# Performance work log

Hardware: AMD Instinct MI355X
Metric: run time of the kernel (lower is better)

Reference implementation:

```python
import jax, jax.numpy as jnp
import numpy as np
from jax import lax

B, T, A = 64, 1024, 512
FILTERS, K = 32, 31
PAD = (K - 1) // 2


def setup_inputs() -> dict:
    key = jax.random.key(0)
    ks = jax.random.split(key, 12)
    return {
        "encoder_seq_proj": jax.random.normal(ks[0], (B, T, A), jnp.float32),
        "query": jax.random.normal(ks[1], (B, A), jnp.float32),
        "cumulative": jax.random.uniform(ks[2], (B, T), jnp.float32),
        "attention": jax.random.uniform(ks[3], (B, T), jnp.float32),
        "alpha": jax.random.uniform(ks[4], (B, T), jnp.float32),
        "conv_w": jax.random.normal(ks[5], (FILTERS, 2, K), jnp.float32) * 0.1,
        "L_w": jax.random.normal(ks[6], (A, FILTERS), jnp.float32) * 0.1,
        "L_b": jax.random.normal(ks[7], (A,), jnp.float32) * 0.1,
        "W_w": jax.random.normal(ks[8], (A, A), jnp.float32) * 0.05,
        "W_b": jax.random.normal(ks[9], (A,), jnp.float32) * 0.05,
        "v_w": jax.random.normal(ks[10], (1, A), jnp.float32) * 0.05,
        "t": 1,
        "phone_len": jax.random.randint(ks[11], (B,), 1, T + 1).astype(jnp.int64),
    }


def reference(encoder_seq_proj, query, cumulative, attention, alpha,
              conv_w, L_w, L_b, W_w, W_b, v_w, t, phone_len):
    # attention mask from phone lengths (set at init, reused each step)
    mask = (jnp.arange(T)[None, :] < phone_len[:, None]).astype(encoder_seq_proj.dtype)
    # processed query: [B, 1, A]
    pq = (query @ W_w.T + W_b)[:, None, :]
    # location features: stack cumulative + previous attention -> [B, 2, T]
    loc = jnp.stack([cumulative, attention], axis=1)
    conv_out = lax.conv_general_dilated(
        loc, conv_w, window_strides=(1,), padding=[(PAD, PAD)],
        dimension_numbers=("NCH", "OIH", "NCH"))  # [B, F, T]
    ploc = jnp.einsum("bft,af->bta", conv_out, L_w) + L_b  # [B, T, A]
    # additive energies -> [B, T]
    u = jnp.einsum("bta,a->bt", jnp.tanh(pq + encoder_seq_proj + ploc), v_w[0])
    s = jax.nn.sigmoid(u)
    scores = s / jnp.sum(s, axis=1, keepdims=True)
    att = scores * mask
    # forward-attention recursion (enable_forward_bias=True path)
    shift_alpha = jnp.pad(alpha[:, :-1], ((0, 0), (1, 0)))
    dual_alpha = jnp.pad(alpha[:, :-2], ((0, 0), (2, 0)))
    new_alpha = (shift_alpha + dual_alpha + alpha + 1e-7) * att
    new_alpha = new_alpha / jnp.sum(new_alpha, axis=-1, keepdims=True)
    return new_alpha[:, None, :]  # [B, 1, T]
```

## Files before the change

### kernel.cpp

```cpp
#include <hip/hip_runtime.h>

#define NB 64
#define NT 1024
#define NA 512
#define NF 32
#define KW 31
#define PADW 15
#define TC 64
#define CWN (2 * KW * NF)

typedef __fp16 half2v __attribute__((ext_vector_type(2)));

__device__ __forceinline__ float fast_tanh(float x) {
    float e = __builtin_amdgcn_exp2f(x * 2.885390081777927f);
    return 1.0f - 2.0f * __builtin_amdgcn_rcpf(1.0f + e);
}
__device__ __forceinline__ float fast_sigmoid(float u) {
    return __builtin_amdgcn_rcpf(1.0f + __builtin_amdgcn_exp2f(-u * 1.4426950408889634f));
}
__device__ __forceinline__ unsigned pkrtz(float a, float b) {
    half2v h = __builtin_amdgcn_cvt_pkrtz(a, b);
    return __builtin_bit_cast(unsigned, h);
}
__device__ __forceinline__ float fdot2u(unsigned cv, unsigned lw, float acc) {
#if __has_builtin(__builtin_amdgcn_fdot2)
    return __builtin_amdgcn_fdot2(__builtin_bit_cast(half2v, cv),
                                  __builtin_bit_cast(half2v, lw), acc, false);
#else
    half2v a = __builtin_bit_cast(half2v, cv), b = __builtin_bit_cast(half2v, lw);
    return acc + (float)a.x * (float)b.x + (float)a.y * (float)b.y;
#endif
}

__global__ __launch_bounds__(256) void lsa_pq(
    const float* __restrict__ query, const float* __restrict__ Ww,
    const float* __restrict__ Wb, const float* __restrict__ convw,
    float* __restrict__ pq, float* __restrict__ cwT)
{
    if (blockIdx.x == 0) {
        for (int i = threadIdx.x; i < NF * 2 * KW; i += 256) {
            int f = i / (2 * KW);
            int r = i - f * 2 * KW;
            int c = r / KW;
            int k = r - c * KW;
            cwT[(c * KW + k) * NF + f] = convw[i];
        }
    }
    __shared__ float qs[NA];
    int tid  = threadIdx.x;
    int lane = tid & 63;
    int wv   = tid >> 6;
    int b     = blockIdx.x >> 3;
    int chunk = blockIdx.x & 7;
    qs[tid]       = query[b * NA + tid];
    qs[tid + 256] = query[b * NA + tid + 256];
    __syncthreads();

    float4 q0 = *(const float4*)(qs + 8 * lane);
    float4 q1 = *(const float4*)(qs + 8 * lane + 4);
#pragma unroll 4
    for (int i = 0; i < 16; ++i) {
        int a = chunk * 64 + wv * 16 + i;
        const float4* wr = (const float4*)(Ww + (long)a * NA + 8 * lane);
        float4 w0 = wr[0], w1 = wr[1];
        float s = w0.x * q0.x + w0.y * q0.y + w0.z * q0.z + w0.w * q0.w
                + w1.x * q1.x + w1.y * q1.y + w1.z * q1.z + w1.w * q1.w;
#pragma unroll
        for (int m = 1; m <= 32; m <<= 1) s += __shfl_xor(s, m, 64);
        if (lane == 0) pq[b * NA + a] = s + Wb[a];
    }
}

__global__ __launch_bounds__(256, 4) void lsa_main(
    const float* __restrict__ enc, const float* __restrict__ cum,
    const float* __restrict__ att, const float* __restrict__ cwT,
    const float* __restrict__ Lw, const float* __restrict__ Lb,
    const float* __restrict__ vw, const float* __restrict__ pq,
    float* __restrict__ sout)
{
    __shared__ float cw_s[CWN];
    __shared__ float cum_s[TC + 30];
    __shared__ float att_s[TC + 30];
    __shared__ unsigned cvsh[TC][20];
    __shared__ float wred[4][34];

    int tid  = threadIdx.x;
    int lane = tid & 63;
    int wv   = tid >> 6;
    int b    = blockIdx.x >> 4;
    int t0   = (blockIdx.x & 15) * TC;

    {
        const float4* src = (const float4*)cwT;
        float4* dst = (float4*)cw_s;
        if (tid < 248) {
            dst[tid]       = src[tid];
            dst[tid + 248] = src[tid + 248];
        }
    }
    if (tid < TC + 30) {
        int t = t0 - PADW + tid;
        bool ok = (t >= 0) && (t < NT);
        cum_s[tid] = ok ? cum[b * NT + t] : 0.f;
        att_s[tid] = ok ? att[b * NT + t] : 0.f;
    }

    int a0  = (tid & 127) * 4;
    int tth = tid >> 7;
    unsigned h[4][16];
    float c4[4], v4[4];
#pragma unroll
    for (int ai = 0; ai < 4; ++ai) {
        const float4* lp = (const float4*)(Lw + (long)(a0 + ai) * NF);
#pragma unroll
        for (int i = 0; i < 8; ++i) {
            float4 w = lp[i];
            h[ai][2 * i]     = pkrtz(w.x, w.y);
            h[ai][2 * i + 1] = pkrtz(w.z, w.w);
        }
        c4[ai] = pq[b * NA + a0 + ai] + Lb[a0 + ai];
        v4[ai] = vw[a0 + ai];
    }
    __syncthreads();

    {
        int tt  = lane;
        int fbu = wv * 8;
        float acc[8] = {0, 0, 0, 0, 0, 0, 0, 0};
#pragma unroll
        for (int k = 0; k < KW; ++k) {
            float x0 = cum_s[tt + k];
            float x1 = att_s[tt + k];
            const float4* A  = (const float4*)(cw_s + k * NF + fbu);
            const float4* Bv = (const float4*)(cw_s + (KW + k) * NF + fbu);
#pragma unroll
            for (int j = 0; j < 2; ++j) {
                float4 wa = A[j], wb = Bv[j];
                acc[4 * j + 0] = fmaf(x0, wa.x, fmaf(x1, wb.x, acc[4 * j + 0]));
                acc[4 * j + 1] = fmaf(x0, wa.y, fmaf(x1, wb.y, acc[4 * j + 1]));
                acc[4 * j + 2] = fmaf(x0, wa.z, fmaf(x1, wb.z, acc[4 * j + 2]));
                acc[4 * j + 3] = fmaf(x0, wa.w, fmaf(x1, wb.w, acc[4 * j + 3]));
            }
        }
        uint4 pk;
        pk.x = pkrtz(acc[0], acc[1]);
        pk.y = pkrtz(acc[2], acc[3]);
        pk.z = pkrtz(acc[4], acc[5]);
        pk.w = pkrtz(acc[6], acc[7]);
        *(uint4*)&cvsh[tt][wv * 4] = pk;
    }
    __syncthreads();

#define DOA(ai, ecomp)                                                  \
    {                                                                   \
        float y0 = 0.f, y1 = 0.f;                                       \
        y0 = fdot2u(cva.x, h[ai][0],  y0); y1 = fdot2u(cva.y, h[ai][1],  y1); \
        y0 = fdot2u(cva.z, h[ai][2],  y0); y1 = fdot2u(cva.w, h[ai][3],  y1); \
        y0 = fdot2u(cvb.x, h[ai][4],  y0); y1 = fdot2u(cvb.y, h[ai][5],  y1); \
        y0 = fdot2u(cvb.z, h[ai][6],  y0); y1 = fdot2u(cvb.w, h[ai][7],  y1); \
        y0 = fdot2u(cvc.x, h[ai][8],  y0); y1 = fdot2u(cvc.y, h[ai][9],  y1); \
        y0 = fdot2u(cvc.z, h[ai][10], y0); y1 = fdot2u(cvc.w, h[ai][11], y1); \
        y0 = fdot2u(cvd.x, h[ai][12], y0); y1 = fdot2u(cvd.y, h[ai][13], y1); \
        y0 = fdot2u(cvd.z, h[ai][14], y0); y1 = fdot2u(cvd.w, h[ai][15], y1); \
        s = fmaf(fast_tanh(y0 + y1 + c4[ai] + (ecomp)), v4[ai], s);     \
    }

    const float* erow = enc + ((long)b * NT + t0 + tth * 32) * NA + a0;
#pragma unroll 1
    for (int g = 0; g < 4; ++g) {
        float p[8];
#pragma unroll
        for (int j = 0; j < 8; ++j) {
            int tt  = g * 8 + j;
            int gtt = tth * 32 + tt;
            float4 e = *(const float4*)(erow + (long)tt * NA);
            uint4 cva = *(const uint4*)&cvsh[gtt][0];
            uint4 cvb = *(const uint4*)&cvsh[gtt][4];
            uint4 cvc = *(const uint4*)&cvsh[gtt][8];
            uint4 cvd = *(const uint4*)&cvsh[gtt][12];
            float s = 0.f;
            DOA(0, e.x)
            DOA(1, e.y)
            DOA(2, e.z)
            DOA(3, e.w)
            p[j] = s;
        }

        {
            int len = 8;
#pragma unroll
            for (int m = 1; m <= 4; m <<= 1) {
                int hlen = len >> 1;
                bool up = (lane & m) != 0;
#pragma unroll
                for (int i = 0; i < 4; ++i) {
                    if (i < hlen) {
                        float send = up ? p[i] : p[i + hlen];
                        float keep = up ? p[i + hlen] : p[i];
                        p[i] = keep + __shfl_xor(send, m, 64);
                    }
                }
                len = hlen;
            }
            float v = p[0];
            v += __shfl_xor(v, 8, 64);
            v += __shfl_xor(v, 16, 64);
            v += __shfl_xor(v, 32, 64);
            int l3 = lane & 7;
            int tt = ((l3 & 1) << 2) | (l3 & 2) | ((l3 & 4) >> 2);
            if (lane < 8) wred[wv][g * 8 + tt] = v;
        }
    }
#undef DOA
    __syncthreads();
    if (tid < TC) {
        float u = (tid < 32) ? (wred[0][tid] + wred[1][tid])
                             : (wred[2][tid - 32] + wred[3][tid - 32]);
        sout[b * NT + t0 + tid] = fast_sigmoid(u);
    }
}

__global__ __launch_bounds__(256) void lsa_norm(
    const float* __restrict__ alpha, const int* __restrict__ plen,
    float* __restrict__ out)
{
    __shared__ float red[4];
    int tid = threadIdx.x;
    int b = blockIdx.x;
    int pl = plen[b];
    float w[4];
    float psum = 0.f;
#pragma unroll
    for (int j = 0; j < 4; ++j) {
        int t = tid + 256 * j;
        float s   = out[b * NT + t];
        float al  = alpha[b * NT + t];
        float am1 = (t >= 1) ? alpha[b * NT + t - 1] : 0.f;
        float am2 = (t >= 2) ? alpha[b * NT + t - 2] : 0.f;
        float val = (t < pl) ? (al + am1 + am2 + 1e-7f) * s : 0.f;
        w[j] = val;
        psum += val;
    }
#pragma unroll
    for (int m = 32; m >= 1; m >>= 1) psum += __shfl_xor(psum, m, 64);
    int lane = tid & 63, wid = tid >> 6;
    if (lane == 0) red[wid] = psum;
    __syncthreads();
    float total = red[0] + red[1] + red[2] + red[3];
    float inv = 1.0f / total;
#pragma unroll
    for (int j = 0; j < 4; ++j) {
        int t = tid + 256 * j;
        out[b * NT + t] = w[j] * inv;
    }
}

extern "C" void kernel_launch(void* const* d_in, const int* in_sizes, int n_in,
                              void* d_out, int out_size, void* d_ws, size_t ws_size,
                              hipStream_t stream)
{
    const float* enc   = (const float*)d_in[0];
    const float* query = (const float*)d_in[1];
    const float* cum   = (const float*)d_in[2];
    const float* att   = (const float*)d_in[3];
    const float* alpha = (const float*)d_in[4];
    const float* convw = (const float*)d_in[5];
    const float* Lw    = (const float*)d_in[6];
    const float* Lb    = (const float*)d_in[7];
    const float* Ww    = (const float*)d_in[8];
    const float* Wb    = (const float*)d_in[9];
    const float* vw    = (const float*)d_in[10];
    const int*   plen  = (const int*)d_in[12];

    float* pq  = (float*)d_ws;
    float* cwT = (float*)d_ws + NB * NA;
    float* sout = (float*)d_out;

    lsa_pq  <<<NB * 8,         256, 0, stream>>>(query, Ww, Wb, convw, pq, cwT);
    lsa_main<<<NB * (NT / TC), 256, 0, stream>>>(enc, cum, att, cwT, Lw, Lb, vw, pq, sout);
    lsa_norm<<<NB,             256, 0, stream>>>(alpha, plen, sout);
}
```

Before: 65.17 us.

## Split attention dim across two blocks per tile, one channel per thread

The main kernel now gives each thread one attention channel instead of four, and splits the 512 channels across two blocks per time tile. The grid doubles and each thread keeps 16 packed L weights in registers instead of 64, so occupancy can rise to 8 blocks per CU. Partial energies from the two halves go to a workspace buffer, and the norm kernel sums them and applies the sigmoid there. The cost is that the 31-tap convolution and the shared-memory setup are redundantly computed twice per tile, and encoder loads become scalar per thread rather than float4.

Result: no change. 66.41 us (+1.9%).

```diff
diff --git a/kernel.cpp b/kernel.cpp
--- a/kernel.cpp
+++ b/kernel.cpp
@@ -8,6 +8,7 @@
 #define PADW 15
 #define TC 64
 #define CWN (2 * KW * NF)
+#define UPART_OFF 34816L
 
 typedef __fp16 half2v __attribute__((ext_vector_type(2)));
 
@@ -71,24 +72,27 @@
     }
 }
 
-__global__ __launch_bounds__(256, 4) void lsa_main(
+__global__ __launch_bounds__(256, 8) void lsa_main(
     const float* __restrict__ enc, const float* __restrict__ cum,
     const float* __restrict__ att, const float* __restrict__ cwT,
     const float* __restrict__ Lw, const float* __restrict__ Lb,
     const float* __restrict__ vw, const float* __restrict__ pq,
-    float* __restrict__ sout)
+    float* __restrict__ upart)
 {
     __shared__ float cw_s[CWN];
     __shared__ float cum_s[TC + 30];
     __shared__ float att_s[TC + 30];
     __shared__ unsigned cvsh[TC][20];
-    __shared__ float wred[4][34];
+    __shared__ float wred[4][TC + 2];
 
     int tid  = threadIdx.x;
     int lane = tid & 63;
     int wv   = tid >> 6;
-    int b    = blockIdx.x >> 4;
-    int t0   = (blockIdx.x & 15) * TC;
+    int bid  = blockIdx.x;
+    int b    = bid >> 5;
+    int t0   = ((bid >> 1) & 15) * TC;
+    int ah   = bid & 1;
+    int a    = ah * 256 + tid;
 
     {
         const float4* src = (const float4*)cwT;
@@ -105,22 +109,16 @@
         att_s[tid] = ok ? att[b * NT + t] : 0.f;
     }
 
-    int a0  = (tid & 127) * 4;
-    int tth = tid >> 7;
-    unsigned h[4][16];
-    float c4[4], v4[4];
-#pragma unroll
-    for (int ai = 0; ai < 4; ++ai) {
-        const float4* lp = (const float4*)(Lw + (long)(a0 + ai) * NF);
-#pragma unroll
-        for (int i = 0; i < 8; ++i) {
-            float4 w = lp[i];
-            h[ai][2 * i]     = pkrtz(w.x, w.y);
-            h[ai][2 * i + 1] = pkrtz(w.z, w.w);
-        }
-        c4[ai] = pq[b * NA + a0 + ai] + Lb[a0 + ai];
-        v4[ai] = vw[a0 + ai];
-    }
+    const float4* lp = (const float4*)(Lw + (long)a * NF);
+    unsigned h[16];
+#pragma unroll
+    for (int i = 0; i < 8; ++i) {
+        float4 w = lp[i];
+        h[2 * i]     = pkrtz(w.x, w.y);
+        h[2 * i + 1] = pkrtz(w.z, w.w);
+    }
+    float c = pq[b * NA + a] + Lb[a];
+    float v = vw[a];
     __syncthreads();
 
     {
@@ -151,39 +149,28 @@
     }
     __syncthreads();
 
-#define DOA(ai, ecomp)                                                  \
-    {                                                                   \
-        float y0 = 0.f, y1 = 0.f;                                       \
-        y0 = fdot2u(cva.x, h[ai][0],  y0); y1 = fdot2u(cva.y, h[ai][1],  y1); \
-        y0 = fdot2u(cva.z, h[ai][2],  y0); y1 = fdot2u(cva.w, h[ai][3],  y1); \
-        y0 = fdot2u(cvb.x, h[ai][4],  y0); y1 = fdot2u(cvb.y, h[ai][5],  y1); \
-        y0 = fdot2u(cvb.z, h[ai][6],  y0); y1 = fdot2u(cvb.w, h[ai][7],  y1); \
-        y0 = fdot2u(cvc.x, h[ai][8],  y0); y1 = fdot2u(cvc.y, h[ai][9],  y1); \
-        y0 = fdot2u(cvc.z, h[ai][10], y0); y1 = fdot2u(cvc.w, h[ai][11], y1); \
-        y0 = fdot2u(cvd.x, h[ai][12], y0); y1 = fdot2u(cvd.y, h[ai][13], y1); \
-        y0 = fdot2u(cvd.z, h[ai][14], y0); y1 = fdot2u(cvd.w, h[ai][15], y1); \
-        s = fmaf(fast_tanh(y0 + y1 + c4[ai] + (ecomp)), v4[ai], s);     \
-    }
-
-    const float* erow = enc + ((long)b * NT + t0 + tth * 32) * NA + a0;
+    const float* ecol = enc + ((long)b * NT + t0) * NA + a;
 #pragma unroll 1
-    for (int g = 0; g < 4; ++g) {
+    for (int pass = 0; pass < 8; ++pass) {
         float p[8];
 #pragma unroll
         for (int j = 0; j < 8; ++j) {
-            int tt  = g * 8 + j;
-            int gtt = tth * 32 + tt;
-            float4 e = *(const float4*)(erow + (long)tt * NA);
-            uint4 cva = *(const uint4*)&cvsh[gtt][0];
-            uint4 cvb = *(const uint4*)&cvsh[gtt][4];
-            uint4 cvc = *(const uint4*)&cvsh[gtt][8];
-            uint4 cvd = *(const uint4*)&cvsh[gtt][12];
-            float s = 0.f;
-            DOA(0, e.x)
-            DOA(1, e.y)
-            DOA(2, e.z)
-            DOA(3, e.w)
-            p[j] = s;
+            int gtt = pass * 8 + j;
+            float e = ecol[(long)gtt * NA];
+            uint4 ca = *(const uint4*)&cvsh[gtt][0];
+            uint4 cb = *(const uint4*)&cvsh[gtt][4];
+            uint4 cc = *(const uint4*)&cvsh[gtt][8];
+            uint4 cd = *(const uint4*)&cvsh[gtt][12];
+            float x0 = 0.f, x1 = 0.f;
+            x0 = fdot2u(ca.x, h[0],  x0); x1 = fdot2u(ca.y, h[1],  x1);
+            x0 = fdot2u(ca.z, h[2],  x0); x1 = fdot2u(ca.w, h[3],  x1);
+            x0 = fdot2u(cb.x, h[4],  x0); x1 = fdot2u(cb.y, h[5],  x1);
+            x0 = fdot2u(cb.z, h[6],  x0); x1 = fdot2u(cb.w, h[7],  x1);
+            x0 = fdot2u(cc.x, h[8],  x0); x1 = fdot2u(cc.y, h[9],  x1);
+            x0 = fdot2u(cc.z, h[10], x0); x1 = fdot2u(cc.w, h[11], x1);
+            x0 = fdot2u(cd.x, h[12], x0); x1 = fdot2u(cd.y, h[13], x1);
+            x0 = fdot2u(cd.z, h[14], x0); x1 = fdot2u(cd.w, h[15], x1);
+            p[j] = fast_tanh(x0 + x1 + c + e) * v;
         }
 
         {
@@ -202,27 +189,25 @@
                 }
                 len = hlen;
             }
-            float v = p[0];
-            v += __shfl_xor(v, 8, 64);
-            v += __shfl_xor(v, 16, 64);
-            v += __shfl_xor(v, 32, 64);
+            float s = p[0];
+            s += __shfl_xor(s, 8, 64);
+            s += __shfl_xor(s, 16, 64);
+            s += __shfl_xor(s, 32, 64);
             int l3 = lane & 7;
             int tt = ((l3 & 1) << 2) | (l3 & 2) | ((l3 & 4) >> 2);
-            if (lane < 8) wred[wv][g * 8 + tt] = v;
-        }
-    }
-#undef DOA
+            if (lane < 8) wred[wv][pass * 8 + tt] = s;
+        }
+    }
     __syncthreads();
     if (tid < TC) {
-        float u = (tid < 32) ? (wred[0][tid] + wred[1][tid])
-                             : (wred[2][tid - 32] + wred[3][tid - 32]);
-        sout[b * NT + t0 + tid] = fast_sigmoid(u);
+        float u = wred[0][tid] + wred[1][tid] + wred[2][tid] + wred[3][tid];
+        upart[((long)ah * NB + b) * NT + t0 + tid] = u;
     }
 }
 
 __global__ __launch_bounds__(256) void lsa_norm(
     const float* __restrict__ alpha, const int* __restrict__ plen,
-    float* __restrict__ out)
+    const float* __restrict__ upart, float* __restrict__ out)
 {
     __shared__ float red[4];
     int tid = threadIdx.x;
@@ -233,7 +218,8 @@
 #pragma unroll
     for (int j = 0; j < 4; ++j) {
         int t = tid + 256 * j;
-        float s   = out[b * NT + t];
+        float u = upart[(long)b * NT + t] + upart[((long)NB + b) * NT + t];
+        float s = fast_sigmoid(u);
         float al  = alpha[b * NT + t];
         float am1 = (t >= 1) ? alpha[b * NT + t - 1] : 0.f;
         float am2 = (t >= 2) ? alpha[b * NT + t - 2] : 0.f;
@@ -272,11 +258,12 @@
     const float* vw    = (const float*)d_in[10];
     const int*   plen  = (const int*)d_in[12];
 
-    float* pq  = (float*)d_ws;
-    float* cwT = (float*)d_ws + NB * NA;
-    float* sout = (float*)d_out;
-
-    lsa_pq  <<<NB * 8,         256, 0, stream>>>(query, Ww, Wb, convw, pq, cwT);
-    lsa_main<<<NB * (NT / TC), 256, 0, stream>>>(enc, cum, att, cwT, Lw, Lb, vw, pq, sout);
-    lsa_norm<<<NB,             256, 0, stream>>>(alpha, plen, sout);
-}
+    float* pq    = (float*)d_ws;
+    float* cwT   = (float*)d_ws + NB * NA;
+    float* upart = (float*)d_ws + UPART_OFF;
+    float* sout  = (float*)d_out;
+
+    lsa_pq  <<<NB * 8,  256, 0, stream>>>(query, Ww, Wb, convw, pq, cwT);
+    lsa_main<<<NB * 32, 256, 0, stream>>>(enc, cum, att, cwT, Lw, Lb, vw, pq, upart);
+    lsa_norm<<<NB,      256, 0, stream>>>(alpha, plen, upart, sout);
+}
```
